# Performance work log

Measured on AMD Instinct MI355X. Metric: run time of the kernel, lower is better.

The kernel has to match this reference:

```python
import math
import jax, jax.numpy as jnp
import numpy as np

N_HEADS = 16
D_KV = 64
NUM_BUCKETS = 32
MAX_DISTANCE = 128


def _relative_position_bucket(relative_position, num_buckets=NUM_BUCKETS, max_distance=MAX_DISTANCE):
    # bidirectional=True (encoder)
    num_buckets //= 2
    n = -relative_position
    ret = (n < 0).astype(jnp.int32) * num_buckets
    n = jnp.abs(n)
    max_exact = num_buckets // 2
    is_small = n < max_exact
    val_if_large = max_exact + (
        jnp.log(jnp.maximum(n, 1).astype(jnp.float32) / max_exact)
        / math.log(max_distance / max_exact)
        * (num_buckets - max_exact)
    ).astype(jnp.int32)
    val_if_large = jnp.minimum(val_if_large, num_buckets - 1)
    return ret + jnp.where(is_small, n, val_if_large)


def setup_inputs() -> dict:
    key = jax.random.key(0)
    ks = jax.random.split(key, 6)
    B, S, D = 2, 2048, 1024
    scale = 0.02  # keep pre-softmax logits in a sane range
    return {
        "x": jax.random.normal(ks[0], (B, S, D), dtype=jnp.float32),
        "Wq": jax.random.normal(ks[1], (D, N_HEADS * D_KV), dtype=jnp.float32) * scale,
        "Wk": jax.random.normal(ks[2], (D, N_HEADS * D_KV), dtype=jnp.float32) * scale,
        "Wv": jax.random.normal(ks[3], (D, N_HEADS * D_KV), dtype=jnp.float32) * scale,
        "Wo": jax.random.normal(ks[4], (N_HEADS * D_KV, D), dtype=jnp.float32) * scale,
        "rel_emb": jax.random.normal(ks[5], (NUM_BUCKETS, N_HEADS), dtype=jnp.float32) * scale,
    }


def reference(x, Wq, Wk, Wv, Wo, rel_emb):
    B, S, D = x.shape
    H, Dk = N_HEADS, D_KV

    def shape(t):  # [B,S,H*Dk] -> [B,H,S,Dk]
        return t.reshape(B, S, H, Dk).transpose(0, 2, 1, 3)

    q = shape(x @ Wq)
    k = shape(x @ Wk)
    v = shape(x @ Wv)

    # NOTE: T5 attention has NO 1/sqrt(d) scaling.
    scores = jnp.einsum("bhqd,bhkd->bhqk", q, k)

    # relative position bias: [1, H, S, S]
    ctx_pos = jnp.arange(S)[:, None]
    mem_pos = jnp.arange(S)[None, :]
    rp_bucket = _relative_position_bucket(mem_pos - ctx_pos)  # [S, S]
    position_bias = rel_emb[rp_bucket].transpose(2, 0, 1)[None]  # [1,H,S,S]

    weights = jax.nn.softmax(scores + position_bias, axis=-1)
    context = jnp.einsum("bhqk,bhkd->bhqd", weights, v)
    context = context.transpose(0, 2, 1, 3).reshape(B, S, H * Dk)
    return context @ Wo
```

## Files before the change

### kernel.cpp

```cpp
#include <hip/hip_runtime.h>
#include <math.h>

typedef unsigned short u16;
typedef unsigned int u32;
typedef __attribute__((ext_vector_type(8))) short bf16x8_t;
typedef __attribute__((ext_vector_type(4))) float f32x4_t;

#define S_LEN  2048
#define NH     16
#define DK     64
#define DMODEL 1024
#define MROWS  4096
#define LOG2E  1.44269504088896f

__device__ inline u16 f2b(float f) {
  union { float f; u32 u; } c; c.f = f;
  u32 u = c.u;
  return (u16)((u + 0x7fffu + ((u >> 16) & 1u)) >> 16);
}

__device__ __forceinline__ float fexp2(float x) {
#if __has_builtin(__builtin_amdgcn_exp2f)
  return __builtin_amdgcn_exp2f(x);
#else
  return exp2f(x);
#endif
}

__device__ __forceinline__ void stage16(const u16* gp_lane, u16* lds_base) {
#if __has_builtin(__builtin_amdgcn_global_load_lds)
  __builtin_amdgcn_global_load_lds((const __attribute__((address_space(1))) u32*)gp_lane,
                                   (__attribute__((address_space(3))) u32*)lds_base, 16, 0, 0);
#else
  *(uint4*)(lds_base + (threadIdx.x & 63) * 8) = *(const uint4*)gp_lane;
#endif
}

__global__ void prep_kernel(const float* __restrict__ x,
                            const float* __restrict__ Wq, const float* __restrict__ Wk,
                            const float* __restrict__ Wv, const float* __restrict__ Wo,
                            const float* __restrict__ rel,
                            u16* __restrict__ xb, u16* __restrict__ Wall,
                            u16* __restrict__ Wto, float* __restrict__ btab) {
  __shared__ float tile[32][33];
  const int bid = blockIdx.x, t = threadIdx.x;
  if (bid < 4096) {
    int i = (bid * 256 + t) * 4;
    float4 v = *(const float4*)(x + i);
    ushort4 o;
    o.x = f2b(v.x); o.y = f2b(v.y); o.z = f2b(v.z); o.w = f2b(v.w);
    *(ushort4*)(xb + i) = o;
  } else if (bid < 8192) {
    int bid2 = bid - 4096;
    int z = bid2 >> 10, rem = bid2 & 1023;
    const float* W; u16* Wt;
    switch (z) {
      case 0: W = Wq; Wt = Wall; break;
      case 1: W = Wk; Wt = Wall + (size_t)DMODEL * DMODEL; break;
      case 2: W = Wv; Wt = Wall + (size_t)2 * DMODEL * DMODEL; break;
      default: W = Wo; Wt = Wto; break;
    }
    int bc = (rem & 31) * 32, br = (rem >> 5) * 32;
    int tx = t & 31, ty = t >> 5;
    #pragma unroll
    for (int yy = 0; yy < 32; yy += 8)
      tile[ty + yy][tx] = W[(size_t)(br + ty + yy) * DMODEL + bc + tx];
    __syncthreads();
    #pragma unroll
    for (int yy = 0; yy < 32; yy += 8)
      Wt[(size_t)(bc + ty + yy) * DMODEL + br + tx] = f2b(tile[tx][ty + yy]);
  } else {
    int idx = (bid - 8192) * 256 + t;
    if (idx < NH * 4095) {
      int h = idx / 4095;
      int dpos = idx - h * 4095;
      int delta = dpos - 2047;
      int ret = (delta > 0) ? 16 : 0;
      int n = delta < 0 ? -delta : delta;
      int bucket;
      if (n < 8) {
        bucket = ret + n;
      } else {
        float vf = logf((float)n * 0.125f) / 2.7725887222397811f * 8.0f;
        int vil = 8 + (int)vf;
        bucket = ret + (vil < 15 ? vil : 15);
      }
      btab[idx] = (rel[bucket * NH + h] - 16.0f) * LOG2E;
    }
  }
}

#define GSTR 56
template <int MODE>
__global__ __launch_bounds__(256) void gemm128_kernel(const u16* __restrict__ A,
                                                      const u16* __restrict__ Bt,
                                                      float* __restrict__ C,
                                                      u16* __restrict__ q16,
                                                      u16* __restrict__ k16,
                                                      u16* __restrict__ vt16) {
  constexpr int ABSZ = (MODE == 1) ? 4608 : 128 * GSTR;
  constexpr int FSTR = (MODE == 1) ? 32 : GSTR;
  __shared__ __align__(16) u16 As[ABSZ];
  __shared__ __align__(16) u16 Bs[ABSZ];
  const int t = threadIdx.x, w = t >> 6, l = t & 63;
  const int c = l & 15, quad = l >> 4;
  const int m0 = blockIdx.x * 128, n0 = blockIdx.y * 128;
  const int wm = (w & 1) * 64, wn = (w >> 1) * 64;

  f32x4_t acc[16] = {};

  if constexpr (MODE == 1) {
    const int sr = l >> 2;
    const int k8 = (l & 3) * 8;
    const u16* Ag0 = A  + (size_t)(m0 + w * 32 + sr) * DMODEL + k8;
    const u16* Ag1 = Ag0 + (size_t)16 * DMODEL;
    const u16* Bg0 = Bt + (size_t)(n0 + w * 32 + sr) * DMODEL + k8;
    const u16* Bg1 = Bg0 + (size_t)16 * DMODEL;
    u16* Al = As + w * 1024;
    u16* Bl = Bs + w * 1024;
    for (int k0 = 0; k0 < DMODEL; k0 += 32) {
      __syncthreads();
      stage16(Ag0 + k0, Al);
      stage16(Ag1 + k0, Al + 512);
      stage16(Bg0 + k0, Bl);
      stage16(Bg1 + k0, Bl + 512);
      __syncthreads();
      bf16x8_t af[4], bfr[4];
      #pragma unroll
      for (int i = 0; i < 4; ++i) {
        af[i]  = *(const bf16x8_t*)(As + (wm + i * 16 + c) * FSTR + quad * 8);
        bfr[i] = *(const bf16x8_t*)(Bs + (wn + i * 16 + c) * FSTR + quad * 8);
      }
      #pragma unroll
      for (int mt = 0; mt < 4; ++mt)
        #pragma unroll
        for (int nt = 0; nt < 4; ++nt)
          acc[mt * 4 + nt] = __builtin_amdgcn_mfma_f32_16x16x32_bf16(af[mt], bfr[nt], acc[mt * 4 + nt], 0, 0, 0);
    }
  } else {
    const int sr = t >> 2;
    const int k8 = (t & 3) * 8;
    const u16* Ag0 = A  + (size_t)(m0 + sr) * DMODEL + k8;
    const u16* Ag1 = Ag0 + (size_t)64 * DMODEL;
    const u16* Bg0 = Bt + (size_t)(n0 + sr) * DMODEL + k8;
    const u16* Bg1 = Bg0 + (size_t)64 * DMODEL;
    u16* Al0 = As + sr * GSTR + k8;
    u16* Al1 = Al0 + 64 * GSTR;
    u16* Bl0 = Bs + sr * GSTR + k8;
    u16* Bl1 = Bl0 + 64 * GSTR;

    uint4 a0 = *(const uint4*)Ag0, a1 = *(const uint4*)Ag1;
    uint4 b0 = *(const uint4*)Bg0, b1 = *(const uint4*)Bg1;
    for (int k0 = 0; k0 < DMODEL; k0 += 32) {
      __syncthreads();
      *(uint4*)Al0 = a0; *(uint4*)Al1 = a1;
      *(uint4*)Bl0 = b0; *(uint4*)Bl1 = b1;
      __syncthreads();
      if (k0 + 32 < DMODEL) {
        a0 = *(const uint4*)(Ag0 + k0 + 32);
        a1 = *(const uint4*)(Ag1 + k0 + 32);
        b0 = *(const uint4*)(Bg0 + k0 + 32);
        b1 = *(const uint4*)(Bg1 + k0 + 32);
      }
      bf16x8_t af[4], bfr[4];
      #pragma unroll
      for (int i = 0; i < 4; ++i) {
        af[i]  = *(const bf16x8_t*)(As + (wm + i * 16 + c) * FSTR + quad * 8);
        bfr[i] = *(const bf16x8_t*)(Bs + (wn + i * 16 + c) * FSTR + quad * 8);
      }
      #pragma unroll
      for (int mt = 0; mt < 4; ++mt)
        #pragma unroll
        for (int nt = 0; nt < 4; ++nt)
          acc[mt * 4 + nt] = __builtin_amdgcn_mfma_f32_16x16x32_bf16(af[mt], bfr[nt], acc[mt * 4 + nt], 0, 0, 0);
    }
  }

  if constexpr (MODE == 0) {
    #pragma unroll
    for (int mt = 0; mt < 4; ++mt) {
      int grow0 = m0 + wm + mt * 16 + quad * 4;
      #pragma unroll
      for (int nt = 0; nt < 4; ++nt) {
        int gcol = n0 + wn + nt * 16 + c;
        #pragma unroll
        for (int r = 0; r < 4; ++r)
          C[(size_t)(grow0 + r) * DMODEL + gcol] = acc[mt * 4 + nt][r];
      }
    }
  } else {
    const int whichblk = n0 >> 10;
    if (whichblk == 2) {
      #pragma unroll
      for (int mt = 0; mt < 4; ++mt) {
        int grow0 = m0 + wm + mt * 16 + quad * 4;
        int b = grow0 >> 11, s0 = grow0 & 2047;
        #pragma unroll
        for (int nt = 0; nt < 4; ++nt) {
          int cc = (n0 + wn + nt * 16 + c) & 1023;
          int hh = cc >> 6, dk = cc & 63;
          f32x4_t v4 = acc[mt * 4 + nt];
          ushort4 o;
          o.x = f2b(v4[0]); o.y = f2b(v4[1]); o.z = f2b(v4[2]); o.w = f2b(v4[3]);
          *(ushort4*)(vt16 + (((size_t)(b * NH + hh)) * DK + dk) * S_LEN + s0) = o;
        }
      }
    } else {
      u16* tb = (w & 1) ? Bs : As;
      const int base_mw = m0 + wm;
      const int bb = base_mw >> 11, s0g = base_mw & 2047;
      const int cc = (n0 + wn) & 1023;
      const int hh = cc >> 6;
      u16* qk = (whichblk == 0 ? q16 : k16) + (((size_t)(bb * NH + hh)) * S_LEN + s0g) * DK;
      __syncthreads();
      #pragma unroll
      for (int round = 0; round < 2; ++round) {
        if ((w >> 1) == round) {
          #pragma unroll
          for (int mt = 0; mt < 4; ++mt)
            #pragma unroll
            for (int nt = 0; nt < 4; ++nt)
              #pragma unroll
              for (int r = 0; r < 4; ++r)
                tb[(mt * 16 + quad * 4 + r) * 72 + nt * 16 + c] = f2b(acc[mt * 4 + nt][r]);
          #pragma unroll
          for (int i = 0; i < 8; ++i) {
            int lrow = i * 8 + (l >> 3);
            int chk = l & 7;
            uint4 vv = *(const uint4*)(tb + lrow * 72 + chk * 8);
            *(uint4*)(qk + (size_t)lrow * DK + chk * 8) = vv;
          }
        }
        __syncthreads();
      }
    }
  }
}

#define ASTR 72
__global__ __launch_bounds__(256) void attn_mfma_kernel(const u16* __restrict__ q,
                                                        const u16* __restrict__ k,
                                                        const u16* __restrict__ vt,
                                                        const float* __restrict__ btab,
                                                        u16* __restrict__ ctx) {
  __shared__ __align__(16) u16 Ks[64 * ASTR];
  __shared__ __align__(16) u16 Vts[64 * ASTR];
  __shared__ __align__(16) u16 Ps[4][16 * ASTR];
  __shared__ float band[192];

  const int t = threadIdx.x;
  const int w = t >> 6, l = t & 63;
  const int c = l & 15, quad = l >> 4;
  const int bh = blockIdx.y;
  const int h = bh & (NH - 1), b = bh >> 4;
  const int q0 = blockIdx.x * 128;

  const u16* qb = q + (size_t)bh * S_LEN * DK;
  const u16* kb = k + (size_t)bh * S_LEN * DK;
  const u16* vb = vt + (size_t)bh * DK * S_LEN;
  const float* btp = btab + h * 4095 + (2047 - 127 - q0);

  bf16x8_t qfrag[2][2];
  #pragma unroll
  for (int qg = 0; qg < 2; ++qg) {
    const u16* qp = qb + (size_t)(q0 + w * 32 + qg * 16 + c) * DK + quad * 8;
    qfrag[qg][0] = *(const bf16x8_t*)(qp);
    qfrag[qg][1] = *(const bf16x8_t*)(qp + 32);
  }

  float lp[2][4] = {};
  f32x4_t O[2][4] = {};

  const int srow = t >> 3;
  const int sc8 = (t & 7) * 8;
  const u16* kg0 = kb + (size_t)srow * DK + sc8;
  const u16* kg1 = kg0 + (size_t)32 * DK;
  const u16* vg0 = vb + (size_t)srow * S_LEN + sc8;
  const u16* vg1 = vg0 + (size_t)32 * S_LEN;
  u16* Kl0 = Ks + srow * ASTR + sc8;
  u16* Kl1 = Kl0 + 32 * ASTR;
  u16* Vl0 = Vts + srow * ASTR + sc8;
  u16* Vl1 = Vl0 + 32 * ASTR;
  u16* Pw = Ps[w];

  uint4 kr0 = *(const uint4*)kg0, kr1 = *(const uint4*)kg1;
  uint4 vr0 = *(const uint4*)vg0, vr1 = *(const uint4*)vg1;
  float br = (t < 192) ? btp[t] : 0.f;

  for (int kt = 0; kt < S_LEN; kt += 64) {
    const int D = kt - q0;
    const bool far = (D >= 256) || (D <= -192);
    *(uint4*)Kl0 = kr0; *(uint4*)Kl1 = kr1;
    *(uint4*)Vl0 = vr0; *(uint4*)Vl1 = vr1;
    if (t < 192) band[t] = br;
    __syncthreads();
    if (kt + 64 < S_LEN) {
      kr0 = *(const uint4*)(kg0 + (size_t)(kt + 64) * DK);
      kr1 = *(const uint4*)(kg1 + (size_t)(kt + 64) * DK);
      vr0 = *(const uint4*)(vg0 + (kt + 64));
      vr1 = *(const uint4*)(vg1 + (kt + 64));
      br = (t < 192) ? btp[kt + 64 + t] : 0.f;
    }

    bf16x8_t kf[2][4];
    #pragma unroll
    for (int kc = 0; kc < 2; ++kc)
      #pragma unroll
      for (int nt = 0; nt < 4; ++nt)
        kf[kc][nt] = *(const bf16x8_t*)(Ks + (nt * 16 + c) * ASTR + kc * 32 + quad * 8);

    f32x4_t s4[2][4] = {};
    #pragma unroll
    for (int qg = 0; qg < 2; ++qg)
      #pragma unroll
      for (int kc = 0; kc < 2; ++kc)
        #pragma unroll
        for (int nt = 0; nt < 4; ++nt)
          s4[qg][nt] = __builtin_amdgcn_mfma_f32_16x16x32_bf16(qfrag[qg][kc], kf[kc][nt], s4[qg][nt], 0, 0, 0);

    bf16x8_t vf[2][4];
    #pragma unroll
    for (int kc = 0; kc < 2; ++kc)
      #pragma unroll
      for (int nt = 0; nt < 4; ++nt)
        vf[kc][nt] = *(const bf16x8_t*)(Vts + (nt * 16 + c) * ASTR + kc * 32 + quad * 8);

    const float bfc = band[127];
    #pragma unroll
    for (int qg = 0; qg < 2; ++qg) {
      const int bnd0 = c - (w * 32 + qg * 16 + quad * 4) + 127;
      if (far) {
        #pragma unroll
        for (int nt = 0; nt < 4; ++nt)
          #pragma unroll
          for (int r = 0; r < 4; ++r) {
            float p = fexp2(fmaf(s4[qg][nt][r], LOG2E, bfc));
            lp[qg][r] += p;
            union { float f; u32 u; } cv; cv.f = p;
            Pw[(quad * 4 + r) * ASTR + nt * 16 + c] = (u16)((cv.u + 0x8000u) >> 16);
          }
      } else {
        #pragma unroll
        for (int nt = 0; nt < 4; ++nt)
          #pragma unroll
          for (int r = 0; r < 4; ++r) {
            float p = fexp2(fmaf(s4[qg][nt][r], LOG2E, band[bnd0 + nt * 16 - r]));
            lp[qg][r] += p;
            union { float f; u32 u; } cv; cv.f = p;
            Pw[(quad * 4 + r) * ASTR + nt * 16 + c] = (u16)((cv.u + 0x8000u) >> 16);
          }
      }
      #pragma unroll
      for (int kc = 0; kc < 2; ++kc) {
        bf16x8_t afr = *(const bf16x8_t*)(Pw + c * ASTR + kc * 32 + quad * 8);
        #pragma unroll
        for (int nt = 0; nt < 4; ++nt)
          O[qg][nt] = __builtin_amdgcn_mfma_f32_16x16x32_bf16(afr, vf[kc][nt], O[qg][nt], 0, 0, 0);
      }
    }
    __syncthreads();
  }

  #pragma unroll
  for (int off = 1; off < 16; off <<= 1)
    #pragma unroll
    for (int qg = 0; qg < 2; ++qg)
      #pragma unroll
      for (int r = 0; r < 4; ++r)
        lp[qg][r] += __shfl_xor(lp[qg][r], off, 64);
  #pragma unroll
  for (int qg = 0; qg < 2; ++qg)
    #pragma unroll
    for (int r = 0; r < 4; ++r) {
      float inv = 1.0f / lp[qg][r];
      int s = q0 + w * 32 + qg * 16 + quad * 4 + r;
      u16* cp = ctx + ((size_t)(b * S_LEN + s)) * DMODEL + h * DK + c;
      #pragma unroll
      for (int nt = 0; nt < 4; ++nt)
        cp[nt * 16] = f2b(O[qg][nt][r] * inv);
    }
}

extern "C" void kernel_launch(void* const* d_in, const int* in_sizes, int n_in,
                              void* d_out, int out_size, void* d_ws, size_t ws_size,
                              hipStream_t stream) {
  const float* x   = (const float*)d_in[0];
  const float* Wq  = (const float*)d_in[1];
  const float* Wk  = (const float*)d_in[2];
  const float* Wv  = (const float*)d_in[3];
  const float* Wo  = (const float*)d_in[4];
  const float* rel = (const float*)d_in[5];
  float* out = (float*)d_out;

  char* ws = (char*)d_ws;
  size_t off = 0;
  auto carve = [&](size_t bytes) -> char* {
    char* p = ws + off;
    off += (bytes + 255) & ~(size_t)255;
    return p;
  };
  u16*   xb   = (u16*)  carve((size_t)MROWS * DMODEL * 2);
  u16*   Wall = (u16*)  carve((size_t)3 * DMODEL * DMODEL * 2);
  u16*   Wto  = (u16*)  carve((size_t)DMODEL * DMODEL * 2);
  u16*   qb16 = (u16*)  carve((size_t)4194304 * 2);
  u16*   kb16 = (u16*)  carve((size_t)4194304 * 2);
  u16*   vt16 = (u16*)  carve((size_t)4194304 * 2);
  float* btab = (float*)carve(((size_t)NH * 4095 + 256) * 4);
  u16*   ctxb = (u16*)  carve((size_t)4194304 * 2);

  prep_kernel<<<8448, 256, 0, stream>>>(x, Wq, Wk, Wv, Wo, rel, xb, Wall, Wto, btab);

  dim3 qkvgrid(32, 24);
  gemm128_kernel<1><<<qkvgrid, 256, 0, stream>>>(xb, Wall, nullptr, qb16, kb16, vt16);

  dim3 agrid(S_LEN / 128, 32);
  attn_mfma_kernel<<<agrid, 256, 0, stream>>>(qb16, kb16, vt16, btab, ctxb);

  dim3 ogrid(32, 8);
  gemm128_kernel<0><<<ogrid, 256, 0, stream>>>(ctxb, Wto, out, nullptr, nullptr, nullptr);
}
```

Before: 197.9 us.

## Use 8 waves per attention block with transposed S=K·Q MFMA and packed P stores

The attention kernel moves from 4 waves handling 32 query rows each to 8 waves handling 16 rows each, with 512 threads per block and a single K/V staging load per thread. The QK MFMA operands are swapped so each lane owns one query column. This lets P be written as packed bf16 pairs with v_cvt_pk_bf16_f32 and lets the row sum be reduced with two shuffles instead of sixteen. The aim is more waves in flight to hide latency and less per-wave register and LDS store work. In exchange, the K/V tiles staged in LDS are now shared by twice as many waves, and the P store pattern changes.

```diff
diff --git a/kernel.cpp b/kernel.cpp
--- a/kernel.cpp
+++ b/kernel.cpp
@@ -238,14 +238,14 @@
 }
 
 #define ASTR 72
-__global__ __launch_bounds__(256) void attn_mfma_kernel(const u16* __restrict__ q,
-                                                        const u16* __restrict__ k,
-                                                        const u16* __restrict__ vt,
-                                                        const float* __restrict__ btab,
-                                                        u16* __restrict__ ctx) {
+__global__ __launch_bounds__(512, 4) void attn_mfma_kernel(const u16* __restrict__ q,
+                                                           const u16* __restrict__ k,
+                                                           const u16* __restrict__ vt,
+                                                           const float* __restrict__ btab,
+                                                           u16* __restrict__ ctx) {
   __shared__ __align__(16) u16 Ks[64 * ASTR];
   __shared__ __align__(16) u16 Vts[64 * ASTR];
-  __shared__ __align__(16) u16 Ps[4][16 * ASTR];
+  __shared__ __align__(16) u16 Ps[8][16 * ASTR];
   __shared__ float band[192];
 
   const int t = threadIdx.x;
@@ -260,125 +260,110 @@
   const u16* vb = vt + (size_t)bh * DK * S_LEN;
   const float* btp = btab + h * 4095 + (2047 - 127 - q0);
 
-  bf16x8_t qfrag[2][2];
-  #pragma unroll
-  for (int qg = 0; qg < 2; ++qg) {
-    const u16* qp = qb + (size_t)(q0 + w * 32 + qg * 16 + c) * DK + quad * 8;
-    qfrag[qg][0] = *(const bf16x8_t*)(qp);
-    qfrag[qg][1] = *(const bf16x8_t*)(qp + 32);
-  }
-
-  float lp[2][4] = {};
-  f32x4_t O[2][4] = {};
+  bf16x8_t qfrag[2];
+  {
+    const u16* qp = qb + (size_t)(q0 + w * 16 + c) * DK + quad * 8;
+    qfrag[0] = *(const bf16x8_t*)(qp);
+    qfrag[1] = *(const bf16x8_t*)(qp + 32);
+  }
+
+  float lp = 0.f;
+  f32x4_t O[4] = {};
 
   const int srow = t >> 3;
   const int sc8 = (t & 7) * 8;
-  const u16* kg0 = kb + (size_t)srow * DK + sc8;
-  const u16* kg1 = kg0 + (size_t)32 * DK;
-  const u16* vg0 = vb + (size_t)srow * S_LEN + sc8;
-  const u16* vg1 = vg0 + (size_t)32 * S_LEN;
-  u16* Kl0 = Ks + srow * ASTR + sc8;
-  u16* Kl1 = Kl0 + 32 * ASTR;
-  u16* Vl0 = Vts + srow * ASTR + sc8;
-  u16* Vl1 = Vl0 + 32 * ASTR;
+  const u16* kg = kb + (size_t)srow * DK + sc8;
+  const u16* vg = vb + (size_t)srow * S_LEN + sc8;
+  u16* Kl = Ks + srow * ASTR + sc8;
+  u16* Vl = Vts + srow * ASTR + sc8;
   u16* Pw = Ps[w];
-
-  uint4 kr0 = *(const uint4*)kg0, kr1 = *(const uint4*)kg1;
-  uint4 vr0 = *(const uint4*)vg0, vr1 = *(const uint4*)vg1;
+  const int qit = w * 16 + c;
+
+  uint4 kr = *(const uint4*)kg;
+  uint4 vr = *(const uint4*)vg;
   float br = (t < 192) ? btp[t] : 0.f;
 
   for (int kt = 0; kt < S_LEN; kt += 64) {
     const int D = kt - q0;
     const bool far = (D >= 256) || (D <= -192);
-    *(uint4*)Kl0 = kr0; *(uint4*)Kl1 = kr1;
-    *(uint4*)Vl0 = vr0; *(uint4*)Vl1 = vr1;
+    *(uint4*)Kl = kr;
+    *(uint4*)Vl = vr;
     if (t < 192) band[t] = br;
     __syncthreads();
     if (kt + 64 < S_LEN) {
-      kr0 = *(const uint4*)(kg0 + (size_t)(kt + 64) * DK);
-      kr1 = *(const uint4*)(kg1 + (size_t)(kt + 64) * DK);
-      vr0 = *(const uint4*)(vg0 + (kt + 64));
-      vr1 = *(const uint4*)(vg1 + (kt + 64));
+      kr = *(const uint4*)(kg + (size_t)(kt + 64) * DK);
+      vr = *(const uint4*)(vg + (kt + 64));
       br = (t < 192) ? btp[kt + 64 + t] : 0.f;
     }
 
-    bf16x8_t kf[2][4];
-    #pragma unroll
-    for (int kc = 0; kc < 2; ++kc)
+    f32x4_t s4[4] = {};
+    #pragma unroll
+    for (int kc = 0; kc < 2; ++kc) {
+      bf16x8_t kf[4];
       #pragma unroll
       for (int nt = 0; nt < 4; ++nt)
-        kf[kc][nt] = *(const bf16x8_t*)(Ks + (nt * 16 + c) * ASTR + kc * 32 + quad * 8);
-
-    f32x4_t s4[2][4] = {};
-    #pragma unroll
-    for (int qg = 0; qg < 2; ++qg)
-      #pragma unroll
-      for (int kc = 0; kc < 2; ++kc)
-        #pragma unroll
-        for (int nt = 0; nt < 4; ++nt)
-          s4[qg][nt] = __builtin_amdgcn_mfma_f32_16x16x32_bf16(qfrag[qg][kc], kf[kc][nt], s4[qg][nt], 0, 0, 0);
-
-    bf16x8_t vf[2][4];
-    #pragma unroll
-    for (int kc = 0; kc < 2; ++kc)
+        kf[nt] = *(const bf16x8_t*)(Ks + (nt * 16 + c) * ASTR + kc * 32 + quad * 8);
       #pragma unroll
       for (int nt = 0; nt < 4; ++nt)
-        vf[kc][nt] = *(const bf16x8_t*)(Vts + (nt * 16 + c) * ASTR + kc * 32 + quad * 8);
-
-    const float bfc = band[127];
-    #pragma unroll
-    for (int qg = 0; qg < 2; ++qg) {
-      const int bnd0 = c - (w * 32 + qg * 16 + quad * 4) + 127;
-      if (far) {
-        #pragma unroll
-        for (int nt = 0; nt < 4; ++nt)
-          #pragma unroll
-          for (int r = 0; r < 4; ++r) {
-            float p = fexp2(fmaf(s4[qg][nt][r], LOG2E, bfc));
-            lp[qg][r] += p;
-            union { float f; u32 u; } cv; cv.f = p;
-            Pw[(quad * 4 + r) * ASTR + nt * 16 + c] = (u16)((cv.u + 0x8000u) >> 16);
-          }
-      } else {
-        #pragma unroll
-        for (int nt = 0; nt < 4; ++nt)
-          #pragma unroll
-          for (int r = 0; r < 4; ++r) {
-            float p = fexp2(fmaf(s4[qg][nt][r], LOG2E, band[bnd0 + nt * 16 - r]));
-            lp[qg][r] += p;
-            union { float f; u32 u; } cv; cv.f = p;
-            Pw[(quad * 4 + r) * ASTR + nt * 16 + c] = (u16)((cv.u + 0x8000u) >> 16);
-          }
-      }
-      #pragma unroll
-      for (int kc = 0; kc < 2; ++kc) {
-        bf16x8_t afr = *(const bf16x8_t*)(Pw + c * ASTR + kc * 32 + quad * 8);
-        #pragma unroll
-        for (int nt = 0; nt < 4; ++nt)
-          O[qg][nt] = __builtin_amdgcn_mfma_f32_16x16x32_bf16(afr, vf[kc][nt], O[qg][nt], 0, 0, 0);
+        s4[nt] = __builtin_amdgcn_mfma_f32_16x16x32_bf16(kf[nt], qfrag[kc], s4[nt], 0, 0, 0);
+    }
+
+    if (far) {
+      const float bfc = band[127];
+      #pragma unroll
+      for (int nt = 0; nt < 4; ++nt) {
+        float p0 = fexp2(fmaf(s4[nt][0], LOG2E, bfc));
+        float p1 = fexp2(fmaf(s4[nt][1], LOG2E, bfc));
+        float p2 = fexp2(fmaf(s4[nt][2], LOG2E, bfc));
+        float p3 = fexp2(fmaf(s4[nt][3], LOG2E, bfc));
+        lp += (p0 + p1) + (p2 + p3);
+        u32 w01, w23;
+        asm("v_cvt_pk_bf16_f32 %0, %1, %2" : "=v"(w01) : "v"(p0), "v"(p1));
+        asm("v_cvt_pk_bf16_f32 %0, %1, %2" : "=v"(w23) : "v"(p2), "v"(p3));
+        *(u32*)(Pw + c * ASTR + nt * 16 + quad * 4)     = w01;
+        *(u32*)(Pw + c * ASTR + nt * 16 + quad * 4 + 2) = w23;
+      }
+    } else {
+      const int bnd0 = 127 + quad * 4 - qit;
+      #pragma unroll
+      for (int nt = 0; nt < 4; ++nt) {
+        float p0 = fexp2(fmaf(s4[nt][0], LOG2E, band[bnd0 + nt * 16 + 0]));
+        float p1 = fexp2(fmaf(s4[nt][1], LOG2E, band[bnd0 + nt * 16 + 1]));
+        float p2 = fexp2(fmaf(s4[nt][2], LOG2E, band[bnd0 + nt * 16 + 2]));
+        float p3 = fexp2(fmaf(s4[nt][3], LOG2E, band[bnd0 + nt * 16 + 3]));
+        lp += (p0 + p1) + (p2 + p3);
+        u32 w01, w23;
+        asm("v_cvt_pk_bf16_f32 %0, %1, %2" : "=v"(w01) : "v"(p0), "v"(p1));
+        asm("v_cvt_pk_bf16_f32 %0, %1, %2" : "=v"(w23) : "v"(p2), "v"(p3));
+        *(u32*)(Pw + c * ASTR + nt * 16 + quad * 4)     = w01;
+        *(u32*)(Pw + c * ASTR + nt * 16 + quad * 4 + 2) = w23;
+      }
+    }
+
+    #pragma unroll
+    for (int kc = 0; kc < 2; ++kc) {
+      bf16x8_t afr = *(const bf16x8_t*)(Pw + c * ASTR + kc * 32 + quad * 8);
+      #pragma unroll
+      for (int nt = 0; nt < 4; ++nt) {
+        bf16x8_t vfr = *(const bf16x8_t*)(Vts + (nt * 16 + c) * ASTR + kc * 32 + quad * 8);
+        O[nt] = __builtin_amdgcn_mfma_f32_16x16x32_bf16(afr, vfr, O[nt], 0, 0, 0);
       }
     }
     __syncthreads();
   }
 
+  lp += __shfl_xor(lp, 16, 64);
+  lp += __shfl_xor(lp, 32, 64);
+
   #pragma unroll
-  for (int off = 1; off < 16; off <<= 1)
-    #pragma unroll
-    for (int qg = 0; qg < 2; ++qg)
-      #pragma unroll
-      for (int r = 0; r < 4; ++r)
-        lp[qg][r] += __shfl_xor(lp[qg][r], off, 64);
-  #pragma unroll
-  for (int qg = 0; qg < 2; ++qg)
-    #pragma unroll
-    for (int r = 0; r < 4; ++r) {
-      float inv = 1.0f / lp[qg][r];
-      int s = q0 + w * 32 + qg * 16 + quad * 4 + r;
-      u16* cp = ctx + ((size_t)(b * S_LEN + s)) * DMODEL + h * DK + c;
-      #pragma unroll
-      for (int nt = 0; nt < 4; ++nt)
-        cp[nt * 16] = f2b(O[qg][nt][r] * inv);
-    }
+  for (int r = 0; r < 4; ++r) {
+    float inv = 1.0f / __shfl(lp, quad * 4 + r, 64);
+    int s = q0 + w * 16 + quad * 4 + r;
+    u16* cp = ctx + ((size_t)(b * S_LEN + s)) * DMODEL + h * DK + c;
+    #pragma unroll
+    for (int nt = 0; nt < 4; ++nt)
+      cp[nt * 16] = f2b(O[nt][r] * inv);
+  }
 }
 
 extern "C" void kernel_launch(void* const* d_in, const int* in_sizes, int n_in,
@@ -414,7 +399,7 @@
   gemm128_kernel<1><<<qkvgrid, 256, 0, stream>>>(xb, Wall, nullptr, qb16, kb16, vt16);
 
   dim3 agrid(S_LEN / 128, 32);
-  attn_mfma_kernel<<<agrid, 256, 0, stream>>>(qb16, kb16, vt16, btab, ctxb);
+  attn_mfma_kernel<<<agrid, 512, 0, stream>>>(qb16, kb16, vt16, btab, ctxb);
 
   dim3 ogrid(32, 8);
   gemm128_kernel<0><<<ogrid, 256, 0, stream>>>(ctxb, Wto, out, nullptr, nullptr, nullptr);
```

New measurement: 194.1 us. No clear change (-1.9%).
